# Performance work log

Hardware: AMD Instinct MI355X
Metric: run time of the kernel (lower is better)

The kernel has to match this reference:

```python
import jax, jax.numpy as jnp
import numpy as np

NPOINT = 1024   # S: number of FPS centroids
RADIUS = 0.15   # ball-query radius
NSAMPLE = 32    # K: neighbors per ball


def setup_inputs() -> dict:
    key = jax.random.key(0)
    ks = jax.random.split(key, 10)
    B, N, C, H = 8, 4096, 64, 128
    xyz = jax.random.uniform(ks[0], (B, N, 3), dtype=jnp.float32)
    features = jax.random.normal(ks[1], (B, N, C), dtype=jnp.float32)
    def dense(k, fan_in, fan_out):
        return jax.random.normal(k, (fan_in, fan_out), dtype=jnp.float32) * (1.0 / np.sqrt(fan_in))
    return {
        "xyz": xyz,
        "features": features,
        "W1f": dense(ks[2], 3 + C, H), "b1f": jnp.zeros((H,), jnp.float32),
        "W2f": dense(ks[3], H, H),     "b2f": jnp.zeros((H,), jnp.float32),
        "W1w": dense(ks[4], 3 + H, H), "b1w": jnp.zeros((H,), jnp.float32),
        "W2w": dense(ks[5], H, H),     "b2w": jnp.zeros((H,), jnp.float32),
    }


def _fps(xyz, npoint):
    """Farthest point sampling. xyz (B,N,3) -> idx (B,npoint). Deterministic start at index 0."""
    B = xyz.shape[0]
    start = jnp.zeros((B,), dtype=jnp.int32)
    centroid = xyz[:, 0, :]                                   # (B,3)
    dist = jnp.sum((xyz - centroid[:, None, :]) ** 2, axis=-1)  # (B,N)

    def step(dist, _):
        far = jnp.argmax(dist, axis=-1).astype(jnp.int32)     # (B,)
        c = jnp.take_along_axis(xyz, far[:, None, None], axis=1)  # (B,1,3)
        dist = jnp.minimum(dist, jnp.sum((xyz - c) ** 2, axis=-1))
        return dist, far

    _, idxs = jax.lax.scan(step, dist, None, length=npoint - 1)  # idxs (npoint-1, B)
    return jnp.concatenate([start[:, None], idxs.T], axis=1)     # (B, npoint)


def _gather(points, idx):
    # points (B,N,C), idx (B,...) int -> (B,...,C)
    return jax.vmap(lambda p, i: p[i])(points, idx)


def reference(xyz, features, W1f, b1f, W2f, b2f, W1w, b1w, W2w, b2w):
    # --- FPS + gather centroids ---
    idx = _fps(xyz, NPOINT)
    new_xyz = _gather(xyz, idx)                               # (B,S,3)
    # --- ball query: full pairwise sq-distance (B,S,N), mask, take nsample nearest ---
    d2 = jnp.sum((new_xyz[:, :, None, :] - xyz[:, None, :, :]) ** 2, axis=-1)
    masked = jnp.where(d2 <= RADIUS ** 2, d2, jnp.inf)
    gidx = jnp.argsort(masked, axis=-1)[:, :, :NSAMPLE]       # (B,S,K)
    # --- group + relative coords ---
    grouped_xyz = _gather(xyz, gidx)                          # (B,S,K,3)
    dxyz = grouped_xyz - new_xyz[:, :, None, :]
    grouped_feats = _gather(features, gidx)                   # (B,S,K,C)
    # --- feature MLP ---
    f_in = jnp.concatenate([dxyz, grouped_feats], axis=-1)    # (B,S,K,3+C)
    f_prime = jax.nn.relu(jax.nn.relu(f_in @ W1f + b1f) @ W2f + b2f)  # (B,S,K,H)
    # --- attention weights + weighted local sum ---
    f_mean = jnp.mean(f_prime, axis=2, keepdims=True)
    w_in = jnp.concatenate([dxyz, f_prime - f_mean], axis=-1) # (B,S,K,3+H)
    alpha = jax.nn.sigmoid(jax.nn.relu(w_in @ W1w + b1w) @ W2w + b2w)
    f_out = jnp.sum(alpha * f_prime, axis=2)                  # (B,S,H)
    return new_xyz, f_out
```

## Files before the change

kernel.cpp:

```cpp
#include <hip/hip_runtime.h>
#include <hip/hip_bf16.h>
#include <stdint.h>

#define NB 8
#define NPTS 4096
#define NPOINT 1024
#define NSAMPLE 32
#define FCH 64
#define HID 128
#define CAPW 160

typedef unsigned long long ull;
typedef __attribute__((ext_vector_type(8))) short short8;
typedef __attribute__((ext_vector_type(4))) float f32x4;

__device__ __forceinline__ float d2_exact(float ax, float ay, float az,
                                          float bx, float by, float bz) {
  float dx = ax - bx, dy = ay - by, dz = az - bz;
  return __fadd_rn(__fadd_rn(__fmul_rn(dx, dx), __fmul_rn(dy, dy)),
                   __fmul_rn(dz, dz));
}

__device__ __forceinline__ unsigned short f2bf(float x) {
  __hip_bfloat16 b = __float2bfloat16(x);
  unsigned short u;
  __builtin_memcpy(&u, &b, 2);
  return u;
}

#define DPPMAX(v, ctrl)                                                     \
  v = fmaxf(v, __int_as_float(__builtin_amdgcn_update_dpp(                  \
                 0, __float_as_int(v), ctrl, 0xf, 0xf, true)))

struct ProdS {
  float4 pts[NPTS];
  float chunk[64 * 3];
  float4 wkd4[2];
  int4 wki4[2];
};
struct ConsS {
  alignas(16) unsigned short a1[32][104];
  alignas(16) unsigned short hbf[32][136];
  float fp32[32][HID];
  float fm[HID];
  float dxyz[32][4];
  int sidx[NSAMPLE];
  int scnt[4];
  int tkS;
  ull candseg[4][CAPW];
  ull cand2[4 * CAPW];
};
union SMemU {
  ProdS p;
  ConsS c;
  unsigned char pad_[86016];
};

__global__ __launch_bounds__(256) void convert_w(const float* __restrict__ W1f,
                                                 const float* __restrict__ W2f,
                                                 const float* __restrict__ W1w,
                                                 const float* __restrict__ W2w,
                                                 unsigned short* __restrict__ wt) {
  int i = blockIdx.x * 256 + threadIdx.x;
  if (i >= 61440) return;
  float v;
  if (i < 12288) {
    int n = i / 96, k = i - n * 96;
    v = (k < 67) ? W1f[k * HID + n] : 0.f;
  } else if (i < 28672) {
    int j = i - 12288;
    int n = j >> 7, k = j & 127;
    v = W2f[k * HID + n];
  } else if (i < 45056) {
    int j = i - 28672;
    int n = j >> 7, k = j & 127;
    v = W1w[(k + 3) * HID + n];
  } else {
    int j = i - 45056;
    int n = j >> 7, k = j & 127;
    v = W2w[k * HID + n];
  }
  wt[i] = f2bf(v);
}

__device__ void run_fps(const float* __restrict__ xyz,
                        float* __restrict__ newxyz, int* progress, int b,
                        ProdS& S) {
  const int t = threadIdx.x;
  const int wid = t >> 6;
  const float* src = xyz + (size_t)b * NPTS * 3;
  float* dstb = newxyz + (size_t)b * NPOINT * 3;
  for (int j = t; j < NPTS; j += 256) {
    const float* p = src + 3 * j;
    S.pts[j] = make_float4(p[0], p[1], p[2], 0.f);
  }
  __syncthreads();
  const int base = t * 16;
  float px[16], py[16], pz[16], dist[16];
  const float4 c0 = S.pts[0];
  float bv = -INFINITY;
  int br = 0;
#pragma unroll
  for (int r = 0; r < 16; ++r) {
    float4 p = S.pts[base + r];
    px[r] = p.x; py[r] = p.y; pz[r] = p.z;
    dist[r] = d2_exact(px[r], py[r], pz[r], c0.x, c0.y, c0.z);
    bool c = dist[r] > bv;
    bv = c ? dist[r] : bv;
    br = c ? r : br;
  }
  if (t == 0) {
    S.chunk[0] = c0.x; S.chunk[1] = c0.y; S.chunk[2] = c0.z;
  }
  for (int it = 1; it < NPOINT; ++it) {
    float wm = bv;
    DPPMAX(wm, 0x111); DPPMAX(wm, 0x112); DPPMAX(wm, 0x114); DPPMAX(wm, 0x118);
    DPPMAX(wm, 0x142); DPPMAX(wm, 0x143);
    float gmaxw =
        __int_as_float(__builtin_amdgcn_readlane(__float_as_int(wm), 63));
    ull m = __ballot(bv == gmaxw);
    int lead = __ffsll((long long)m) - 1;
    int widx = __builtin_amdgcn_readlane(base + br, lead);
    const int par = it & 1;
    if ((t & 63) == 0) {
      ((float*)&S.wkd4[par])[wid] = gmaxw;
      ((int*)&S.wki4[par])[wid] = widx;
    }
    __syncthreads();
    if ((it & 63) == 0) {
      if (t < 192) {
        dstb[(it - 64) * 3 + t] = S.chunk[t];
        __threadfence();
      }
      __syncthreads();
      if (t == 0)
        __hip_atomic_store(&progress[b], it, __ATOMIC_RELEASE,
                           __HIP_MEMORY_SCOPE_AGENT);
    }
    float4 dd = S.wkd4[par];
    int4 ii = S.wki4[par];
    float d = dd.x; int fi = ii.x;
    bool c1 = (dd.y > d) || (dd.y == d && ii.y < fi);
    d = c1 ? dd.y : d; fi = c1 ? ii.y : fi;
    bool c2 = (dd.z > d) || (dd.z == d && ii.z < fi);
    d = c2 ? dd.z : d; fi = c2 ? ii.z : fi;
    bool c3 = (dd.w > d) || (dd.w == d && ii.w < fi);
    fi = c3 ? ii.w : fi;
    const float4 cp = S.pts[fi];
    if (t == 0) {
      int slot = (it & 63) * 3;
      S.chunk[slot + 0] = cp.x;
      S.chunk[slot + 1] = cp.y;
      S.chunk[slot + 2] = cp.z;
    }
    bv = -INFINITY;
    br = 0;
#pragma unroll
    for (int r = 0; r < 16; ++r) {
      float dnew = d2_exact(px[r], py[r], pz[r], cp.x, cp.y, cp.z);
      float nd = fminf(dist[r], dnew);
      dist[r] = nd;
      bool c = nd > bv;
      bv = c ? nd : bv;
      br = c ? r : br;
    }
  }
  __syncthreads();
  if (t < 192) {
    dstb[(NPOINT - 64) * 3 + t] = S.chunk[t];
    __threadfence();
  }
  __syncthreads();
  if (t == 0)
    __hip_atomic_store(&progress[b], NPOINT, __ATOMIC_RELEASE,
                       __HIP_MEMORY_SCOPE_AGENT);
}

__device__ __forceinline__ void mfma_tiles(const unsigned short* __restrict__ A,
                                           int lda,
                                           const unsigned short* __restrict__ WT,
                                           int ldw, int ksteps, int wv,
                                           int lane, f32x4 acc[4]) {
  const int mi = lane & 15;
  const int qo = (lane >> 4) * 8;
#pragma unroll
  for (int i = 0; i < 4; ++i) {
    const int m = (i & 1) * 16 + mi;
    const int n = (wv * 2 + (i >> 1)) * 16 + mi;
    f32x4 a = {0.f, 0.f, 0.f, 0.f};
    for (int ks = 0; ks < ksteps; ++ks) {
      short8 af = *(const short8*)(A + (size_t)m * lda + ks * 32 + qo);
      short8 bf = *(const short8*)(WT + (size_t)n * ldw + ks * 32 + qo);
      a = __builtin_amdgcn_mfma_f32_16x16x32_bf16(af, bf, a, 0, 0, 0);
    }
    acc[i] = a;
  }
}

__device__ void run_consumer(const float* __restrict__ xyz,
                             const float* __restrict__ feats,
                             const unsigned short* __restrict__ wt,
                             const float* __restrict__ b1f,
                             const float* __restrict__ b2f,
                             const float* __restrict__ W1w,
                             const float* __restrict__ b1w,
                             const float* __restrict__ b2w,
                             const float* __restrict__ newxyz,
                             float* __restrict__ fout, int* progress,
                             int* ticket, ConsS& S) {
  const int t = threadIdx.x;
  const int wv = t >> 6;
  const int lane = t & 63;
  const float r2 = 0.0225f;
  const unsigned short* WT1f = wt;
  const unsigned short* WT2f = wt + 12288;
  const unsigned short* WT1w = wt + 28672;
  const unsigned short* WT2w = wt + 45056;

  for (int e = t; e < 32 * 104 / 2; e += 256) ((unsigned int*)S.a1)[e] = 0u;
  __syncthreads();

  while (true) {
    if (t == 0) S.tkS = atomicAdd(ticket, 1);
    __syncthreads();
    const int tk = S.tkS;
    if (tk >= NB * NPOINT) return;
    const int it = tk >> 3;
    const int b = tk & 7;
    const int g = b * NPOINT + it;

    if (t == 0) {
      while (__hip_atomic_load(&progress[b], __ATOMIC_RELAXED,
                               __HIP_MEMORY_SCOPE_AGENT) <= it)
        __builtin_amdgcn_s_sleep(32);
    }
    __syncthreads();
    {
      int pv = __hip_atomic_load(&progress[b], __ATOMIC_ACQUIRE,
                                 __HIP_MEMORY_SCOPE_AGENT);
      while (pv <= it) {
        __builtin_amdgcn_s_sleep(8);
        pv = __hip_atomic_load(&progress[b], __ATOMIC_ACQUIRE,
                               __HIP_MEMORY_SCOPE_AGENT);
      }
    }
    const float cx = newxyz[g * 3 + 0];
    const float cy = newxyz[g * 3 + 1];
    const float cz = newxyz[g * 3 + 2];

    const float* src = xyz + (size_t)b * NPTS * 3;
    int cnt = 0;
    const int jb = wv * 1024;
    for (int j0 = jb; j0 < jb + 1024; j0 += 64) {
      const int p = j0 + lane;
      const float* pp = src + p * 3;
      float d2 = d2_exact(pp[0], pp[1], pp[2], cx, cy, cz);
      bool inr = (d2 <= r2);
      ull mask = __ballot(inr);
      if (inr) {
        int pos = cnt + __popcll(mask & ((1ull << lane) - 1ull));
        if (pos < CAPW)
          S.candseg[wv][pos] = ((ull)__float_as_uint(d2) << 32) | (unsigned)p;
      }
      cnt += __popcll(mask);
    }
    if (lane == 0) S.scnt[wv] = cnt < CAPW ? cnt : CAPW;
    __syncthreads();
    const int n0 = S.scnt[0], n1 = S.scnt[1], n2 = S.scnt[2], n3 = S.scnt[3];
    const int C = n0 + n1 + n2 + n3;
    {
      int off = (wv > 0 ? n0 : 0) + (wv > 1 ? n1 : 0) + (wv > 2 ? n2 : 0);
      int myn = S.scnt[wv];
      for (int i = lane; i < myn; i += 64) S.cand2[off + i] = S.candseg[wv][i];
    }
    __syncthreads();
    for (int tt = t; tt < C; tt += 256) {
      ull key = S.cand2[tt];
      int rank = 0;
      for (int u = 0; u < C; ++u) rank += (S.cand2[u] < key) ? 1 : 0;
      if (rank < NSAMPLE) S.sidx[rank] = (int)(key & 0xffffffffu);
    }
    if (C < NSAMPLE && wv == 0) {
      const float* pp = src + lane * 3;
      float d2 = d2_exact(pp[0], pp[1], pp[2], cx, cy, cz);
      bool outr = !(d2 <= r2);
      ull mask = __ballot(outr);
      if (outr) {
        int pos = __popcll(mask & ((1ull << lane) - 1ull));
        if (pos < NSAMPLE - C) S.sidx[C + pos] = lane;
      }
    }
    __syncthreads();

    if (t < 32) {
      const float* pp = src + (size_t)S.sidx[t] * 3;
      float dx = pp[0] - cx, dy = pp[1] - cy, dz = pp[2] - cz;
      S.dxyz[t][0] = dx; S.dxyz[t][1] = dy; S.dxyz[t][2] = dz;
      S.dxyz[t][3] = 0.f;
      S.a1[t][0] = f2bf(dx); S.a1[t][1] = f2bf(dy); S.a1[t][2] = f2bf(dz);
    }
    for (int e = t; e < 32 * FCH; e += 256) {
      int s = e >> 6;
      int c = e & 63;
      S.a1[s][3 + c] = f2bf(feats[((size_t)b * NPTS + S.sidx[s]) * FCH + c]);
    }
    __syncthreads();

    f32x4 acc[4];
    const int coli = lane & 15;
    const int rq = (lane >> 4) << 2;

    mfma_tiles(&S.a1[0][0], 104, WT1f, 96, 3, wv, lane, acc);
#pragma unroll
    for (int i = 0; i < 4; ++i) {
      int col = (wv * 2 + (i >> 1)) * 16 + coli;
      float bb = b1f[col];
      int rowb = (i & 1) * 16 + rq;
#pragma unroll
      for (int r = 0; r < 4; ++r)
        S.hbf[rowb + r][col] = f2bf(fmaxf(acc[i][r] + bb, 0.f));
    }
    __syncthreads();

    mfma_tiles(&S.hbf[0][0], 136, WT2f, 128, 4, wv, lane, acc);
#pragma unroll
    for (int i = 0; i < 4; ++i) {
      int col = (wv * 2 + (i >> 1)) * 16 + coli;
      float bb = b2f[col];
      int rowb = (i & 1) * 16 + rq;
#pragma unroll
      for (int r = 0; r < 4; ++r)
        S.fp32[rowb + r][col] = fmaxf(acc[i][r] + bb, 0.f);
    }
    __syncthreads();

    if (t < HID) {
      float s = 0.f;
#pragma unroll 8
      for (int i = 0; i < 32; ++i) s += S.fp32[i][t];
      S.fm[t] = s * (1.0f / 32.0f);
    }
    __syncthreads();

    for (int e = t; e < 32 * HID; e += 256) {
      int s = e >> 7;
      int c = e & 127;
      S.hbf[s][c] = f2bf(S.fp32[s][c] - S.fm[c]);
    }
    __syncthreads();

    mfma_tiles(&S.hbf[0][0], 136, WT1w, 128, 4, wv, lane, acc);
    float h2v[4][4];
#pragma unroll
    for (int i = 0; i < 4; ++i) {
      int col = (wv * 2 + (i >> 1)) * 16 + coli;
      float bb = b1w[col];
      float w0 = W1w[col], w1 = W1w[HID + col], w2 = W1w[2 * HID + col];
      int rowb = (i & 1) * 16 + rq;
#pragma unroll
      for (int r = 0; r < 4; ++r) {
        float4 dz = *(const float4*)S.dxyz[rowb + r];
        h2v[i][r] =
            fmaxf(acc[i][r] + bb + dz.x * w0 + dz.y * w1 + dz.z * w2, 0.f);
      }
    }
    __syncthreads();
#pragma unroll
    for (int i = 0; i < 4; ++i) {
      int col = (wv * 2 + (i >> 1)) * 16 + coli;
      int rowb = (i & 1) * 16 + rq;
#pragma unroll
      for (int r = 0; r < 4; ++r) S.hbf[rowb + r][col] = f2bf(h2v[i][r]);
    }
    __syncthreads();

    mfma_tiles(&S.hbf[0][0], 136, WT2w, 128, 4, wv, lane, acc);
    {
      float psA = 0.f, psB = 0.f;
#pragma unroll
      for (int i = 0; i < 4; ++i) {
        int col = (wv * 2 + (i >> 1)) * 16 + coli;
        float bb = b2w[col];
        int rowb = (i & 1) * 16 + rq;
        float part = 0.f;
#pragma unroll
        for (int r = 0; r < 4; ++r) {
          float al = 1.0f / (1.0f + __expf(-(acc[i][r] + bb)));
          part += al * S.fp32[rowb + r][col];
        }
        if (i < 2) psA += part; else psB += part;
      }
      psA += __shfl_xor(psA, 16);
      psA += __shfl_xor(psA, 32);
      psB += __shfl_xor(psB, 16);
      psB += __shfl_xor(psB, 32);
      if (lane < 16) {
        fout[(size_t)g * HID + wv * 32 + lane] = psA;
        fout[(size_t)g * HID + wv * 32 + 16 + lane] = psB;
      }
    }
    __syncthreads();
  }
}

__global__ __launch_bounds__(256, 1) void sa_fused_kernel(
    const float* __restrict__ xyz, const float* __restrict__ feats,
    const unsigned short* __restrict__ wt, const float* __restrict__ b1f,
    const float* __restrict__ b2f, const float* __restrict__ W1w,
    const float* __restrict__ b1w, const float* __restrict__ b2w,
    float* __restrict__ newxyz, float* __restrict__ fout, int* ctrl) {
  __shared__ SMemU sm;
  int* progress = ctrl;
  int* ticket = ctrl + 8;
  if (blockIdx.x < NB) {
    run_fps(xyz, newxyz, progress, blockIdx.x, sm.p);
    __syncthreads();
  }
  run_consumer(xyz, feats, wt, b1f, b2f, W1w, b1w, b2w, newxyz, fout,
               progress, ticket, sm.c);
}

extern "C" void kernel_launch(void* const* d_in, const int* in_sizes, int n_in,
                              void* d_out, int out_size, void* d_ws, size_t ws_size,
                              hipStream_t stream) {
  const float* xyz = (const float*)d_in[0];
  const float* feats = (const float*)d_in[1];
  const float* W1f = (const float*)d_in[2];
  const float* b1f = (const float*)d_in[3];
  const float* W2f = (const float*)d_in[4];
  const float* b2f = (const float*)d_in[5];
  const float* W1w = (const float*)d_in[6];
  const float* b1w = (const float*)d_in[7];
  const float* W2w = (const float*)d_in[8];
  const float* b2w = (const float*)d_in[9];

  float* newxyz = (float*)d_out;
  float* fout = (float*)d_out + (size_t)NB * NPOINT * 3;
  int* ctrl = (int*)d_ws;
  unsigned short* wt = (unsigned short*)((char*)d_ws + 256);

  hipMemsetAsync(ctrl, 0, 64, stream);
  convert_w<<<240, 256, 0, stream>>>(W1f, W2f, W1w, W2w, wt);
  sa_fused_kernel<<<256, 256, 0, stream>>>(xyz, feats, wt, b1f, b2f, W1w,
                                           b1w, b2w, newxyz, fout, ctrl);
}
```

Baseline: 881.7 us.

## Batch four centroids per consumer work item to enlarge MLP GEMM tiles

Each consumer ticket now handles four centroids instead of one. The ball-query scan loads each point once and tests it against all four centroids, and the per-centroid ranking is split so each wave handles one centroid. The MLP GEMMs run on 128-row tiles, with weight fragments held in registers and reused across eight M tiles, which amortises weight loads and barriers. To fit in shared memory, the first-layer features are stored as bf16 (fpbf) instead of fp32 and several buffers are aliased. This adds rounding error to the mean and weighted sum, raises register pressure, and makes each ticket wait for FPS to finish four centroids.

```diff
diff --git a/kernel.cpp b/kernel.cpp
--- a/kernel.cpp
+++ b/kernel.cpp
@@ -9,6 +9,7 @@
 #define FCH 64
 #define HID 128
 #define CAPW 160
+#define NQ 4
 
 typedef unsigned long long ull;
 typedef __attribute__((ext_vector_type(8))) short short8;
@@ -26,6 +27,9 @@
   unsigned short u;
   __builtin_memcpy(&u, &b, 2);
   return u;
+}
+__device__ __forceinline__ float bf2f(unsigned short u) {
+  return __uint_as_float(((unsigned)u) << 16);
 }
 
 #define DPPMAX(v, ctrl)                                                     \
@@ -39,16 +43,20 @@
   int4 wki4[2];
 };
 struct ConsS {
-  alignas(16) unsigned short a1[32][104];
-  alignas(16) unsigned short hbf[32][136];
-  float fp32[32][HID];
-  float fm[HID];
-  float dxyz[32][4];
-  int sidx[NSAMPLE];
-  int scnt[4];
+  union {
+    unsigned short a1[128][104];
+    unsigned short fpbf[128][136];
+    ull cand2[NQ][4 * CAPW];
+  };
+  union {
+    unsigned short hbf[128][136];
+    ull candseg[4][NQ][CAPW];
+  };
+  float fm[NQ][HID];
+  float dxyz[128][4];
+  int sidx[128];
+  int scnt[4][NQ];
   int tkS;
-  ull candseg[4][CAPW];
-  ull cand2[4 * CAPW];
 };
 union SMemU {
   ProdS p;
@@ -176,24 +184,37 @@
                        __HIP_MEMORY_SCOPE_AGENT);
 }
 
-__device__ __forceinline__ void mfma_tiles(const unsigned short* __restrict__ A,
-                                           int lda,
-                                           const unsigned short* __restrict__ WT,
-                                           int ldw, int ksteps, int wv,
-                                           int lane, f32x4 acc[4]) {
+template <int KSTEPS>
+__device__ __forceinline__ void mfma_gemm128(
+    const unsigned short* __restrict__ A, int lda,
+    const unsigned short* __restrict__ WT, int ldw, int wv, int lane,
+    f32x4 acc[8][2]) {
   const int mi = lane & 15;
   const int qo = (lane >> 4) * 8;
-#pragma unroll
-  for (int i = 0; i < 4; ++i) {
-    const int m = (i & 1) * 16 + mi;
-    const int n = (wv * 2 + (i >> 1)) * 16 + mi;
-    f32x4 a = {0.f, 0.f, 0.f, 0.f};
-    for (int ks = 0; ks < ksteps; ++ks) {
-      short8 af = *(const short8*)(A + (size_t)m * lda + ks * 32 + qo);
-      short8 bf = *(const short8*)(WT + (size_t)n * ldw + ks * 32 + qo);
-      a = __builtin_amdgcn_mfma_f32_16x16x32_bf16(af, bf, a, 0, 0, 0);
-    }
-    acc[i] = a;
+  short8 bfr[2][KSTEPS];
+#pragma unroll
+  for (int ntl = 0; ntl < 2; ++ntl) {
+    const int n = (wv * 2 + ntl) * 16 + mi;
+#pragma unroll
+    for (int ks = 0; ks < KSTEPS; ++ks)
+      bfr[ntl][ks] = *(const short8*)(WT + (size_t)n * ldw + ks * 32 + qo);
+  }
+#pragma unroll
+  for (int mt = 0; mt < 8; ++mt) {
+    const int m = mt * 16 + mi;
+    short8 af[KSTEPS];
+#pragma unroll
+    for (int ks = 0; ks < KSTEPS; ++ks)
+      af[ks] = *(const short8*)(A + (size_t)m * lda + ks * 32 + qo);
+#pragma unroll
+    for (int ntl = 0; ntl < 2; ++ntl) {
+      f32x4 a = acc[mt][ntl];
+#pragma unroll
+      for (int ks = 0; ks < KSTEPS; ++ks)
+        a = __builtin_amdgcn_mfma_f32_16x16x32_bf16(af[ks], bfr[ntl][ks], a,
+                                                    0, 0, 0);
+      acc[mt][ntl] = a;
+    }
   }
 }
 
@@ -217,187 +238,253 @@
   const unsigned short* WT1w = wt + 28672;
   const unsigned short* WT2w = wt + 45056;
 
-  for (int e = t; e < 32 * 104 / 2; e += 256) ((unsigned int*)S.a1)[e] = 0u;
-  __syncthreads();
-
   while (true) {
     if (t == 0) S.tkS = atomicAdd(ticket, 1);
     __syncthreads();
     const int tk = S.tkS;
-    if (tk >= NB * NPOINT) return;
-    const int it = tk >> 3;
+    if (tk >= NB * NPOINT / NQ) return;
+    const int i4 = tk >> 3;
     const int b = tk & 7;
-    const int g = b * NPOINT + it;
+    const int it0 = NQ * i4;
+    const int g0 = b * NPOINT + it0;
 
     if (t == 0) {
       while (__hip_atomic_load(&progress[b], __ATOMIC_RELAXED,
-                               __HIP_MEMORY_SCOPE_AGENT) <= it)
+                               __HIP_MEMORY_SCOPE_AGENT) <= it0 + NQ - 1)
         __builtin_amdgcn_s_sleep(32);
     }
     __syncthreads();
     {
       int pv = __hip_atomic_load(&progress[b], __ATOMIC_ACQUIRE,
                                  __HIP_MEMORY_SCOPE_AGENT);
-      while (pv <= it) {
+      while (pv <= it0 + NQ - 1) {
         __builtin_amdgcn_s_sleep(8);
         pv = __hip_atomic_load(&progress[b], __ATOMIC_ACQUIRE,
                                __HIP_MEMORY_SCOPE_AGENT);
       }
     }
-    const float cx = newxyz[g * 3 + 0];
-    const float cy = newxyz[g * 3 + 1];
-    const float cz = newxyz[g * 3 + 2];
-
     const float* src = xyz + (size_t)b * NPTS * 3;
-    int cnt = 0;
+    float cxa[NQ], cya[NQ], cza[NQ];
+#pragma unroll
+    for (int q = 0; q < NQ; ++q) {
+      cxa[q] = newxyz[(g0 + q) * 3 + 0];
+      cya[q] = newxyz[(g0 + q) * 3 + 1];
+      cza[q] = newxyz[(g0 + q) * 3 + 2];
+    }
+
+    int cnt[NQ] = {0, 0, 0, 0};
     const int jb = wv * 1024;
     for (int j0 = jb; j0 < jb + 1024; j0 += 64) {
       const int p = j0 + lane;
       const float* pp = src + p * 3;
-      float d2 = d2_exact(pp[0], pp[1], pp[2], cx, cy, cz);
-      bool inr = (d2 <= r2);
-      ull mask = __ballot(inr);
-      if (inr) {
-        int pos = cnt + __popcll(mask & ((1ull << lane) - 1ull));
-        if (pos < CAPW)
-          S.candseg[wv][pos] = ((ull)__float_as_uint(d2) << 32) | (unsigned)p;
-      }
-      cnt += __popcll(mask);
-    }
-    if (lane == 0) S.scnt[wv] = cnt < CAPW ? cnt : CAPW;
-    __syncthreads();
-    const int n0 = S.scnt[0], n1 = S.scnt[1], n2 = S.scnt[2], n3 = S.scnt[3];
-    const int C = n0 + n1 + n2 + n3;
+      float x = pp[0], y = pp[1], z = pp[2];
+#pragma unroll
+      for (int q = 0; q < NQ; ++q) {
+        float d2 = d2_exact(x, y, z, cxa[q], cya[q], cza[q]);
+        bool inr = (d2 <= r2);
+        ull mask = __ballot(inr);
+        if (inr) {
+          int pos = cnt[q] + __popcll(mask & ((1ull << lane) - 1ull));
+          if (pos < CAPW)
+            S.candseg[wv][q][pos] =
+                ((ull)__float_as_uint(d2) << 32) | (unsigned)p;
+        }
+        cnt[q] += __popcll(mask);
+      }
+    }
+    if (lane == 0) {
+#pragma unroll
+      for (int q = 0; q < NQ; ++q)
+        S.scnt[wv][q] = cnt[q] < CAPW ? cnt[q] : CAPW;
+    }
+    __syncthreads();
     {
-      int off = (wv > 0 ? n0 : 0) + (wv > 1 ? n1 : 0) + (wv > 2 ? n2 : 0);
-      int myn = S.scnt[wv];
-      for (int i = lane; i < myn; i += 64) S.cand2[off + i] = S.candseg[wv][i];
-    }
-    __syncthreads();
-    for (int tt = t; tt < C; tt += 256) {
-      ull key = S.cand2[tt];
-      int rank = 0;
-      for (int u = 0; u < C; ++u) rank += (S.cand2[u] < key) ? 1 : 0;
-      if (rank < NSAMPLE) S.sidx[rank] = (int)(key & 0xffffffffu);
-    }
-    if (C < NSAMPLE && wv == 0) {
-      const float* pp = src + lane * 3;
-      float d2 = d2_exact(pp[0], pp[1], pp[2], cx, cy, cz);
-      bool outr = !(d2 <= r2);
-      ull mask = __ballot(outr);
-      if (outr) {
-        int pos = __popcll(mask & ((1ull << lane) - 1ull));
-        if (pos < NSAMPLE - C) S.sidx[C + pos] = lane;
-      }
-    }
-    __syncthreads();
-
-    if (t < 32) {
+      const int q = wv;
+      const int n0 = S.scnt[0][q], n1 = S.scnt[1][q], n2 = S.scnt[2][q],
+                n3 = S.scnt[3][q];
+      const int C = n0 + n1 + n2 + n3;
+      int off = 0;
+#pragma unroll
+      for (int w = 0; w < 4; ++w) {
+        int n = S.scnt[w][q];
+        for (int i = lane; i < n; i += 64)
+          S.cand2[q][off + i] = S.candseg[w][q][i];
+        off += n;
+      }
+      __builtin_amdgcn_wave_barrier();
+      for (int tt = lane; tt < C; tt += 64) {
+        ull key = S.cand2[q][tt];
+        int rank = 0;
+        for (int u = 0; u < C; ++u) rank += (S.cand2[q][u] < key) ? 1 : 0;
+        if (rank < NSAMPLE) S.sidx[q * NSAMPLE + rank] = (int)(key & 0xffffffffu);
+      }
+      if (C < NSAMPLE) {
+        const float* pp = src + lane * 3;
+        float d2 = d2_exact(pp[0], pp[1], pp[2], cxa[q], cya[q], cza[q]);
+        bool outr = !(d2 <= r2);
+        ull mask = __ballot(outr);
+        if (outr) {
+          int pos = __popcll(mask & ((1ull << lane) - 1ull));
+          if (pos < NSAMPLE - C) S.sidx[q * NSAMPLE + C + pos] = lane;
+        }
+      }
+    }
+    __syncthreads();
+
+    {
+      int r = t >> 1, half = t & 1;
+      unsigned int* rowp = (unsigned int*)&S.a1[r][68];
+#pragma unroll
+      for (int j = 0; j < 9; ++j) rowp[9 * half + j] = 0u;
+    }
+    if (t < 128) {
+      const int q = t >> 5;
       const float* pp = src + (size_t)S.sidx[t] * 3;
-      float dx = pp[0] - cx, dy = pp[1] - cy, dz = pp[2] - cz;
+      float dx = pp[0] - cxa[q], dy = pp[1] - cya[q], dz = pp[2] - cza[q];
       S.dxyz[t][0] = dx; S.dxyz[t][1] = dy; S.dxyz[t][2] = dz;
       S.dxyz[t][3] = 0.f;
       S.a1[t][0] = f2bf(dx); S.a1[t][1] = f2bf(dy); S.a1[t][2] = f2bf(dz);
-    }
-    for (int e = t; e < 32 * FCH; e += 256) {
+      S.a1[t][67] = 0;
+    }
+    for (int e = t; e < 128 * FCH; e += 256) {
       int s = e >> 6;
       int c = e & 63;
       S.a1[s][3 + c] = f2bf(feats[((size_t)b * NPTS + S.sidx[s]) * FCH + c]);
     }
     __syncthreads();
 
-    f32x4 acc[4];
+    f32x4 acc[8][2];
     const int coli = lane & 15;
     const int rq = (lane >> 4) << 2;
 
-    mfma_tiles(&S.a1[0][0], 104, WT1f, 96, 3, wv, lane, acc);
-#pragma unroll
-    for (int i = 0; i < 4; ++i) {
-      int col = (wv * 2 + (i >> 1)) * 16 + coli;
+#pragma unroll
+    for (int mt = 0; mt < 8; ++mt)
+#pragma unroll
+      for (int ntl = 0; ntl < 2; ++ntl) acc[mt][ntl] = {0.f, 0.f, 0.f, 0.f};
+    mfma_gemm128<3>(&S.a1[0][0], 104, WT1f, 96, wv, lane, acc);
+#pragma unroll
+    for (int ntl = 0; ntl < 2; ++ntl) {
+      int col = (wv * 2 + ntl) * 16 + coli;
       float bb = b1f[col];
-      int rowb = (i & 1) * 16 + rq;
-#pragma unroll
-      for (int r = 0; r < 4; ++r)
-        S.hbf[rowb + r][col] = f2bf(fmaxf(acc[i][r] + bb, 0.f));
-    }
-    __syncthreads();
-
-    mfma_tiles(&S.hbf[0][0], 136, WT2f, 128, 4, wv, lane, acc);
-#pragma unroll
-    for (int i = 0; i < 4; ++i) {
-      int col = (wv * 2 + (i >> 1)) * 16 + coli;
+#pragma unroll
+      for (int mt = 0; mt < 8; ++mt) {
+        int rowb = mt * 16 + rq;
+#pragma unroll
+        for (int r = 0; r < 4; ++r)
+          S.hbf[rowb + r][col] = f2bf(fmaxf(acc[mt][ntl][r] + bb, 0.f));
+      }
+    }
+    __syncthreads();
+
+#pragma unroll
+    for (int mt = 0; mt < 8; ++mt)
+#pragma unroll
+      for (int ntl = 0; ntl < 2; ++ntl) acc[mt][ntl] = {0.f, 0.f, 0.f, 0.f};
+    mfma_gemm128<4>(&S.hbf[0][0], 136, WT2f, 128, wv, lane, acc);
+#pragma unroll
+    for (int ntl = 0; ntl < 2; ++ntl) {
+      int col = (wv * 2 + ntl) * 16 + coli;
       float bb = b2f[col];
-      int rowb = (i & 1) * 16 + rq;
-#pragma unroll
-      for (int r = 0; r < 4; ++r)
-        S.fp32[rowb + r][col] = fmaxf(acc[i][r] + bb, 0.f);
-    }
-    __syncthreads();
-
-    if (t < HID) {
+#pragma unroll
+      for (int mt = 0; mt < 8; ++mt) {
+        int rowb = mt * 16 + rq;
+#pragma unroll
+        for (int r = 0; r < 4; ++r)
+          S.fpbf[rowb + r][col] = f2bf(fmaxf(acc[mt][ntl][r] + bb, 0.f));
+      }
+    }
+    __syncthreads();
+
+    for (int e = t; e < NQ * HID; e += 256) {
+      int q = e >> 7, c = e & 127;
       float s = 0.f;
 #pragma unroll 8
-      for (int i = 0; i < 32; ++i) s += S.fp32[i][t];
-      S.fm[t] = s * (1.0f / 32.0f);
-    }
-    __syncthreads();
-
-    for (int e = t; e < 32 * HID; e += 256) {
-      int s = e >> 7;
-      int c = e & 127;
-      S.hbf[s][c] = f2bf(S.fp32[s][c] - S.fm[c]);
-    }
-    __syncthreads();
-
-    mfma_tiles(&S.hbf[0][0], 136, WT1w, 128, 4, wv, lane, acc);
-    float h2v[4][4];
-#pragma unroll
-    for (int i = 0; i < 4; ++i) {
-      int col = (wv * 2 + (i >> 1)) * 16 + coli;
+      for (int i = 0; i < 32; ++i) s += bf2f(S.fpbf[q * 32 + i][c]);
+      S.fm[q][c] = s * (1.0f / 32.0f);
+    }
+    __syncthreads();
+
+    for (int e = t; e < 128 * 64; e += 256) {
+      int s = e >> 6, j = e & 63;
+      int q = s >> 5;
+      unsigned int pairv = *(unsigned int*)&S.fpbf[s][2 * j];
+      float lo = bf2f((unsigned short)(pairv & 0xffff)) - S.fm[q][2 * j];
+      float hi = bf2f((unsigned short)(pairv >> 16)) - S.fm[q][2 * j + 1];
+      unsigned int outp = (unsigned int)f2bf(lo) | ((unsigned int)f2bf(hi) << 16);
+      *(unsigned int*)&S.hbf[s][2 * j] = outp;
+    }
+    __syncthreads();
+
+#pragma unroll
+    for (int mt = 0; mt < 8; ++mt)
+#pragma unroll
+      for (int ntl = 0; ntl < 2; ++ntl) acc[mt][ntl] = {0.f, 0.f, 0.f, 0.f};
+    mfma_gemm128<4>(&S.hbf[0][0], 136, WT1w, 128, wv, lane, acc);
+#pragma unroll
+    for (int ntl = 0; ntl < 2; ++ntl) {
+      int col = (wv * 2 + ntl) * 16 + coli;
       float bb = b1w[col];
       float w0 = W1w[col], w1 = W1w[HID + col], w2 = W1w[2 * HID + col];
-      int rowb = (i & 1) * 16 + rq;
-#pragma unroll
-      for (int r = 0; r < 4; ++r) {
-        float4 dz = *(const float4*)S.dxyz[rowb + r];
-        h2v[i][r] =
-            fmaxf(acc[i][r] + bb + dz.x * w0 + dz.y * w1 + dz.z * w2, 0.f);
-      }
-    }
-    __syncthreads();
-#pragma unroll
-    for (int i = 0; i < 4; ++i) {
-      int col = (wv * 2 + (i >> 1)) * 16 + coli;
-      int rowb = (i & 1) * 16 + rq;
-#pragma unroll
-      for (int r = 0; r < 4; ++r) S.hbf[rowb + r][col] = f2bf(h2v[i][r]);
-    }
-    __syncthreads();
-
-    mfma_tiles(&S.hbf[0][0], 136, WT2w, 128, 4, wv, lane, acc);
+#pragma unroll
+      for (int mt = 0; mt < 8; ++mt) {
+        int rowb = mt * 16 + rq;
+#pragma unroll
+        for (int r = 0; r < 4; ++r) {
+          float4 dz = *(const float4*)S.dxyz[rowb + r];
+          acc[mt][ntl][r] = fmaxf(
+              acc[mt][ntl][r] + bb + dz.x * w0 + dz.y * w1 + dz.z * w2, 0.f);
+        }
+      }
+    }
+    __syncthreads();
+#pragma unroll
+    for (int ntl = 0; ntl < 2; ++ntl) {
+      int col = (wv * 2 + ntl) * 16 + coli;
+#pragma unroll
+      for (int mt = 0; mt < 8; ++mt) {
+        int rowb = mt * 16 + rq;
+#pragma unroll
+        for (int r = 0; r < 4; ++r)
+          S.hbf[rowb + r][col] = f2bf(acc[mt][ntl][r]);
+      }
+    }
+    __syncthreads();
+
+#pragma unroll
+    for (int mt = 0; mt < 8; ++mt)
+#pragma unroll
+      for (int ntl = 0; ntl < 2; ++ntl) acc[mt][ntl] = {0.f, 0.f, 0.f, 0.f};
+    mfma_gemm128<4>(&S.hbf[0][0], 136, WT2w, 128, wv, lane, acc);
     {
-      float psA = 0.f, psB = 0.f;
-#pragma unroll
-      for (int i = 0; i < 4; ++i) {
-        int col = (wv * 2 + (i >> 1)) * 16 + coli;
+      float ps[NQ][2];
+#pragma unroll
+      for (int q = 0; q < NQ; ++q) { ps[q][0] = 0.f; ps[q][1] = 0.f; }
+#pragma unroll
+      for (int ntl = 0; ntl < 2; ++ntl) {
+        int col = (wv * 2 + ntl) * 16 + coli;
         float bb = b2w[col];
-        int rowb = (i & 1) * 16 + rq;
-        float part = 0.f;
-#pragma unroll
-        for (int r = 0; r < 4; ++r) {
-          float al = 1.0f / (1.0f + __expf(-(acc[i][r] + bb)));
-          part += al * S.fp32[rowb + r][col];
+#pragma unroll
+        for (int mt = 0; mt < 8; ++mt) {
+          int rowb = mt * 16 + rq;
+          float part = 0.f;
+#pragma unroll
+          for (int r = 0; r < 4; ++r) {
+            float al = 1.0f / (1.0f + __expf(-(acc[mt][ntl][r] + bb)));
+            part += al * bf2f(S.fpbf[rowb + r][col]);
+          }
+          ps[mt >> 1][ntl] += part;
         }
-        if (i < 2) psA += part; else psB += part;
-      }
-      psA += __shfl_xor(psA, 16);
-      psA += __shfl_xor(psA, 32);
-      psB += __shfl_xor(psB, 16);
-      psB += __shfl_xor(psB, 32);
-      if (lane < 16) {
-        fout[(size_t)g * HID + wv * 32 + lane] = psA;
-        fout[(size_t)g * HID + wv * 32 + 16 + lane] = psB;
-      }
+      }
+#pragma unroll
+      for (int q = 0; q < NQ; ++q)
+#pragma unroll
+        for (int ntl = 0; ntl < 2; ++ntl) {
+          float v = ps[q][ntl];
+          v += __shfl_xor(v, 16);
+          v += __shfl_xor(v, 32);
+          if (lane < 16)
+            fout[(size_t)(g0 + q) * HID + (wv * 2 + ntl) * 16 + lane] = v;
+        }
     }
     __syncthreads();
   }
```

Measured after the change: 798.3 us. 1.1x faster.
